# Performance work log

Hardware: AMD Instinct MI355X
Metric: run time of the kernel (lower is better)

Reference implementation:

```python
import jax, jax.numpy as jnp
import numpy as np
import math

D_MODEL = 1024
NUM_HEADS = 16
HEAD_DIM = D_MODEL // NUM_HEADS
THETA = 10000.0
B, S = 2, 2048


def _rope(x, positions, theta):
    # x: (b, h, s, d); positions: (s,) int
    d = x.shape[-1]
    inv_freq = theta ** (-jnp.arange(0, d, 2, dtype=jnp.float32) / d)  # (d/2,)
    ang = positions.astype(jnp.float32)[:, None] * inv_freq[None, :]   # (s, d/2)
    cos, sin = jnp.cos(ang), jnp.sin(ang)
    x1 = x[..., ::2]
    x2 = x[..., 1::2]
    r1 = x1 * cos - x2 * sin
    r2 = x1 * sin + x2 * cos
    # interleave back to (..., d)
    return jnp.stack([r1, r2], axis=-1).reshape(x.shape)


def setup_inputs() -> dict:
    key = jax.random.key(0)
    ks = jax.random.split(key, 5)
    std = math.sqrt(2.0 / (D_MODEL + D_MODEL))
    return {
        "x": jax.random.normal(ks[0], (B, S, D_MODEL), dtype=jnp.float32),
        "token_positions": jnp.arange(S, dtype=jnp.int32),
        "Wq": jax.random.normal(ks[1], (D_MODEL, D_MODEL), dtype=jnp.float32) * std,
        "Wk": jax.random.normal(ks[2], (D_MODEL, D_MODEL), dtype=jnp.float32) * std,
        "Wv": jax.random.normal(ks[3], (D_MODEL, D_MODEL), dtype=jnp.float32) * std,
        "Wo": jax.random.normal(ks[4], (D_MODEL, D_MODEL), dtype=jnp.float32) * std,
    }


def reference(x, token_positions, Wq, Wk, Wv, Wo):
    b, s, _ = x.shape
    def split_heads(t):
        return t.reshape(b, s, NUM_HEADS, HEAD_DIM).transpose(0, 2, 1, 3)  # (b,h,s,d)
    Q = split_heads(x @ Wq.T)
    K = split_heads(x @ Wk.T)
    V = split_heads(x @ Wv.T)
    Q = _rope(Q, token_positions, THETA)
    K = _rope(K, token_positions, THETA)
    scores = jnp.einsum("bhqd,bhkd->bhqk", Q, K) / math.sqrt(HEAD_DIM)
    causal = jnp.tril(jnp.ones((s, s), dtype=bool))
    scores = jnp.where(causal, scores, -jnp.inf)
    attn = jax.nn.softmax(scores, axis=-1)
    out = jnp.einsum("bhqk,bhkd->bhqd", attn, V)
    out = out.transpose(0, 2, 1, 3).reshape(b, s, D_MODEL)
    return out @ Wo.T
```

## Files before the change

### kernel.cpp

```cpp
#include <hip/hip_runtime.h>
#include <math.h>

typedef unsigned short u16;
typedef unsigned int   u32;
typedef __attribute__((ext_vector_type(8))) short bf16x8;
typedef __attribute__((ext_vector_type(4))) float floatx4;
typedef __attribute__((ext_vector_type(4))) _Float16 halfx4;
typedef __attribute__((ext_vector_type(2))) unsigned int uintx2;

#define SEQ 2048
#define DM  1024
#define NH  16
#define DH  64
#define MM  4096
#define QSCALE 0.18033688011112042f

__device__ __forceinline__ u16 f2bf(float f) {
    u32 u = __builtin_bit_cast(u32, f);
    u += 0x7fffu + ((u >> 16) & 1u);
    return (u16)(u >> 16);
}

__device__ __forceinline__ void async16(const void* g, void* l) {
    __builtin_amdgcn_global_load_lds(
        (const __attribute__((address_space(1))) void*)g,
        (__attribute__((address_space(3))) void*)l, 16, 0, 0);
}

__global__ __launch_bounds__(256) void prep_kernel(const float* __restrict__ x,
                                                   const float* __restrict__ w0,
                                                   const float* __restrict__ w1,
                                                   const float* __restrict__ w2,
                                                   const float* __restrict__ w3,
                                                   u16* __restrict__ Xsh,
                                                   u16* __restrict__ Wsh,
                                                   const int* __restrict__ pos,
                                                   float2* __restrict__ tab) {
    const int bid = blockIdx.x, cb = blockIdx.y, tid = threadIdx.x;

    int lin = bid * 16 + cb;
    if (lin < 256) {
        int i = lin * 256 + tid;
        int p = i >> 5, d2 = i & 31;
        float freq = __expf(-(float)d2 * (9.2103403719761836f / 32.0f));
        float sv, cv;
        sincosf((float)pos[p] * freq, &sv, &cv);
        tab[i] = make_float2(cv, sv);
    }

    const float* src; u16* dst; int row0;
    if (bid < 64) { src = x; dst = Xsh; row0 = bid * 64; }
    else {
        int wi = (bid - 64) >> 4;
        src = (wi == 0) ? w0 : (wi == 1) ? w1 : (wi == 2) ? w2 : w3;
        dst = Wsh + (size_t)wi * DM * DM;
        row0 = ((bid - 64) & 15) * 64;
    }
    __shared__ __align__(16) u16 t[64 * 64];
#pragma unroll
    for (int rep = 0; rep < 4; ++rep) {
        int f = rep * 256 + tid;
        int r = f >> 4, c4 = f & 15;
        float4 v = *(const float4*)&src[(size_t)(row0 + r) * DM + cb * 64 + c4 * 4];
        uint2 pk;
        pk.x = (u32)f2bf(v.x) | ((u32)f2bf(v.y) << 16);
        pk.y = (u32)f2bf(v.z) | ((u32)f2bf(v.w) << 16);
        int ch = (c4 >> 1) ^ (r & 7);
        *(uint2*)&t[r * 64 + ch * 8 + (c4 & 1) * 4] = pk;
    }
    __syncthreads();
#pragma unroll
    for (int rep = 0; rep < 2; ++rep) {
        int s = rep * 256 + tid;
        int tile = s >> 6, l = s & 63;
        int mt = tile >> 1, kt = tile & 1, lm = l & 15, quad = l >> 4;
        int m = mt * 16 + lm;
        uint4 v = *(const uint4*)&t[m * 64 + ((kt * 4 + quad) ^ (m & 7)) * 8];
        size_t rowblk = (size_t)(row0 >> 4) + mt;
        size_t ktile  = cb * 2 + kt;
        *(uint4*)&dst[(rowblk * 32 + ktile) * 512 + l * 8] = v;
    }
}

template<int MREP, bool OUTF32>
__global__ __launch_bounds__(256, (MREP == 4) ? 3 : 2)
void gemm_s(const u16* __restrict__ Ash,
            const u16* __restrict__ Wbase,
            u16* __restrict__ qout,
            float* __restrict__ outf,
            _Float16* __restrict__ vtout,
            u16* __restrict__ kout,
            const float2* __restrict__ ropetab) {
    constexpr int BM  = MREP * 32;
    constexpr int AC  = 2 * MREP;
    constexpr int APW = AC / 4;
    constexpr int STEP = (AC + 8) * 512;
    constexpr int SHN  = (MREP == 4) ? (128 * 136) : (2 * STEP);

    const int z  = blockIdx.z;
    const u16* Wp = Wbase + (size_t)z * (DM * DM);
    const int m0 = blockIdx.x * BM, n0 = blockIdx.y * 128;
    const int tid = threadIdx.x, lane = tid & 63, w = tid >> 6;
    const int wr = w >> 1, wc = w & 1;
    const int lm = lane & 15, quad = lane >> 4;
    const int rb0 = m0 >> 4, cb0 = n0 >> 4;

    __shared__ __align__(16) u16 sh[SHN];

    auto stage = [&](int buf, int it) {
        u16* la = sh + buf * STEP;
        u16* lb = la + AC * 512;
#pragma unroll
        for (int j = 0; j < APW; ++j) {
            int c = w * APW + j;
            async16(Ash + ((size_t)(rb0 + c) * 32 + it) * 512 + lane * 8,
                    &la[c * 512 + lane * 8]);
        }
#pragma unroll
        for (int j = 0; j < 2; ++j) {
            int c = w * 2 + j;
            async16(Wp + ((size_t)(cb0 + c) * 32 + it) * 512 + lane * 8,
                    &lb[c * 512 + lane * 8]);
        }
    };

    floatx4 acc[MREP][4];
    const floatx4 z4 = {0.f, 0.f, 0.f, 0.f};
#pragma unroll
    for (int mt = 0; mt < MREP; ++mt)
#pragma unroll
        for (int nt = 0; nt < 4; ++nt) acc[mt][nt] = z4;

    stage(0, 0);
    __syncthreads();

#pragma unroll 2
    for (int it = 0; it < 32; ++it) {
        if (it < 31) stage((it + 1) & 1, it + 1);
        const u16* la = sh + (it & 1) * STEP;
        const u16* lb = la + AC * 512;
        bf16x8 a[MREP], b[4];
#pragma unroll
        for (int mt = 0; mt < MREP; ++mt)
            a[mt] = *(const bf16x8*)&la[(wr * MREP + mt) * 512 + lane * 8];
#pragma unroll
        for (int nt = 0; nt < 4; ++nt)
            b[nt] = *(const bf16x8*)&lb[(wc * 4 + nt) * 512 + lane * 8];
#pragma unroll
        for (int mt = 0; mt < MREP; ++mt)
#pragma unroll
            for (int nt = 0; nt < 4; ++nt)
                acc[mt][nt] = __builtin_amdgcn_mfma_f32_16x16x32_bf16(
                    a[mt], b[nt], acc[mt][nt], 0, 0, 0);
        __syncthreads();
    }

    if constexpr (OUTF32) {
#pragma unroll
        for (int mt = 0; mt < MREP; ++mt)
#pragma unroll
            for (int r = 0; r < 4; ++r) {
                int row = m0 + wr * (MREP * 16) + mt * 16 + quad * 4 + r;
#pragma unroll
                for (int nt = 0; nt < 4; ++nt) {
                    int col = n0 + wc * 64 + nt * 16 + lm;
                    outf[(size_t)row * DM + col] = acc[mt][nt][r];
                }
            }
        return;
    } else {
        if (z == 0) {
#pragma unroll
            for (int mt = 0; mt < MREP; ++mt)
#pragma unroll
                for (int r = 0; r < 4; ++r) {
                    int row = m0 + wr * (MREP * 16) + mt * 16 + quad * 4 + r;
#pragma unroll
                    for (int nt = 0; nt < 4; ++nt) {
                        int col = n0 + wc * 64 + nt * 16 + lm;
                        float v  = acc[mt][nt][r];
                        float pv = __shfl_xor(v, 1);
                        float2 cs = ropetab[(row & (SEQ - 1)) * 32 + ((col & 63) >> 1)];
                        v = (lm & 1) ? fmaf(pv, cs.y, v * cs.x) : fmaf(v, cs.x, -pv * cs.y);
                        v *= QSCALE;
                        float hv = __shfl_xor(v, 1);
                        if (!(lm & 1)) {
                            u32 pk = (u32)f2bf(v) | ((u32)f2bf(hv) << 16);
                            *(u32*)&qout[(size_t)row * DM + col] = pk;
                        }
                    }
                }
        } else if (z == 1) {
            if constexpr (MREP == 4) {
                u16* t = sh;
#pragma unroll
                for (int mt = 0; mt < MREP; ++mt)
#pragma unroll
                    for (int r = 0; r < 4; ++r) {
                        int rl  = wr * 64 + mt * 16 + quad * 4 + r;
                        int row = m0 + rl;
#pragma unroll
                        for (int nt = 0; nt < 4; ++nt) {
                            int cl  = wc * 64 + nt * 16 + lm;
                            int col = n0 + cl;
                            float v  = acc[mt][nt][r];
                            float pv = __shfl_xor(v, 1);
                            float2 cs = ropetab[(row & (SEQ - 1)) * 32 + ((col & 63) >> 1)];
                            v = (lm & 1) ? fmaf(pv, cs.y, v * cs.x) : fmaf(v, cs.x, -pv * cs.y);
                            t[rl * 136 + cl] = f2bf(v);
                        }
                    }
                __syncthreads();
                {
                    int bb = m0 >> 11;
                    int sblk0 = (m0 & (SEQ - 1)) >> 4;
                    int h0 = n0 >> 6;
#pragma unroll
                    for (int j = 0; j < 8; ++j) {
                        int c = w * 8 + j;
                        int hloc = c >> 4, sblkl = (c >> 1) & 7, ks2 = c & 1;
                        uint4 v4 = *(const uint4*)&t[(sblkl * 16 + lm) * 136 + hloc * 64 + ks2 * 32 + quad * 8];
                        size_t chunk = ((size_t)(bb * NH + h0 + hloc) * 128 + sblk0 + sblkl) * 2 + ks2;
                        *(uint4*)&kout[chunk * 512 + lane * 8] = v4;
                    }
                }
            }
        } else {
            if constexpr (MREP == 4) {
#pragma unroll
                for (int mt = 0; mt < MREP; ++mt) {
                    int row = m0 + wr * 64 + mt * 16;
                    int b = row >> 11;
                    int sblk = (row & (SEQ - 1)) >> 4;
#pragma unroll
                    for (int nt = 0; nt < 4; ++nt) {
                        int col = n0 + wc * 64 + nt * 16;
                        int h = col >> 6;
                        int dblk = (col & 63) >> 4;
                        size_t chunk = ((size_t)(b * NH + h) * 128 + sblk) * 4 + dblk;
                        uint2 pk;
                        pk.x = __builtin_bit_cast(u32, __builtin_amdgcn_cvt_pkrtz(acc[mt][nt][0], acc[mt][nt][1]));
                        pk.y = __builtin_bit_cast(u32, __builtin_amdgcn_cvt_pkrtz(acc[mt][nt][2], acc[mt][nt][3]));
                        *(uint2*)&vtout[chunk * 256 + lane * 4] = pk;
                    }
                }
            }
        }
    }
}

__global__ __launch_bounds__(256, 2) void attn_kernel(const u16* __restrict__ Q,
                                                      const u16* __restrict__ Kf,
                                                      const _Float16* __restrict__ Vf,
                                                      u16* __restrict__ AO) {
    const int u  = blockIdx.x;
    const int qt = (u < 256) ? (15 - (u >> 5)) : ((u >> 5) - 8);
    const int bh = u & 31;
    const int b  = bh >> 4, h = bh & 15;
    const int q0 = qt * 128;
    const int tid = threadIdx.x, w = tid >> 6, lane = tid & 63;
    const int lm = lane & 15, quad = lane >> 4;

    __shared__ __align__(16) u16      lsK[2][16 * 512];
    __shared__ __align__(16) _Float16 lsV[2][32 * 256];

    bf16x8 qb[2][2];
#pragma unroll
    for (int qi = 0; qi < 2; ++qi)
#pragma unroll
        for (int ks = 0; ks < 2; ++ks)
            qb[qi][ks] = *(const bf16x8*)
                &Q[(size_t)(b * SEQ + q0 + w * 32 + qi * 16 + lm) * DM + h * DH + ks * 32 + quad * 8];

    const floatx4 z4 = {0.f, 0.f, 0.f, 0.f};
    floatx4 o[2][4];
    floatx4 o5[2];
#pragma unroll
    for (int qi = 0; qi < 2; ++qi) {
#pragma unroll
        for (int dt = 0; dt < 4; ++dt) o[qi][dt] = z4;
        o5[qi] = z4;
    }

    const u16*      Kb = Kf + (size_t)bh * (256 * 512);
    const _Float16* Vb = Vf + (size_t)bh * (128 * 4 * 256);

    auto stageKV = [&](int buf, int kt) {
#pragma unroll
        for (int j = 0; j < 4; ++j) {
            int kc = w * 4 + j;
            async16(Kb + ((size_t)kt * 16 + kc) * 512 + lane * 8,
                    &lsK[buf][kc * 512 + lane * 8]);
            int off = w * 2048 + j * 512 + lane * 8;
            async16(Vb + (size_t)kt * 8192 + off, &lsV[buf][off]);
        }
    };

    stageKV(0, 0);
    const halfx4 ones = {(_Float16)1.f, (_Float16)1.f, (_Float16)1.f, (_Float16)1.f};

    for (int kt = 0; kt <= qt; ++kt) {
        __syncthreads();
        if (kt < qt) stageKV((kt + 1) & 1, kt + 1);
        const u16*      Lk = lsK[kt & 1];
        const _Float16* Lv = lsV[kt & 1];

        floatx4 s4[2][8];
#pragma unroll
        for (int qi = 0; qi < 2; ++qi)
#pragma unroll
            for (int st = 0; st < 8; ++st) s4[qi][st] = z4;
#pragma unroll
        for (int ks = 0; ks < 2; ++ks)
#pragma unroll
            for (int st = 0; st < 8; ++st) {
                bf16x8 ka = *(const bf16x8*)&Lk[(st * 2 + ks) * 512 + lane * 8];
#pragma unroll
                for (int qi = 0; qi < 2; ++qi)
                    s4[qi][st] = __builtin_amdgcn_mfma_f32_16x16x32_bf16(ka, qb[qi][ks], s4[qi][st], 0, 0, 0);
            }

        const bool diag = (kt == qt);
#pragma unroll
        for (int st = 0; st < 8; ++st) {
            halfx4 pb2[2];
#pragma unroll
            for (int qi = 0; qi < 2; ++qi) {
#pragma unroll
                for (int r = 0; r < 4; ++r) {
                    float v = s4[qi][st][r];
                    if (diag) {
                        int keyloc = st * 16 + quad * 4 + r;
                        if (keyloc > w * 32 + qi * 16 + lm) v = -1e30f;
                    }
                    s4[qi][st][r] = exp2f(v);
                }
                uintx2 pk2;
                pk2.x = __builtin_bit_cast(u32, __builtin_amdgcn_cvt_pkrtz(s4[qi][st][0], s4[qi][st][1]));
                pk2.y = __builtin_bit_cast(u32, __builtin_amdgcn_cvt_pkrtz(s4[qi][st][2], s4[qi][st][3]));
                pb2[qi] = __builtin_bit_cast(halfx4, pk2);
            }
#pragma unroll
            for (int dt = 0; dt < 4; ++dt) {
                halfx4 va = *(const halfx4*)&Lv[(st * 4 + dt) * 256 + lane * 4];
#pragma unroll
                for (int qi = 0; qi < 2; ++qi)
                    o[qi][dt] = __builtin_amdgcn_mfma_f32_16x16x16f16(va, pb2[qi], o[qi][dt], 0, 0, 0);
            }
#pragma unroll
            for (int qi = 0; qi < 2; ++qi)
                o5[qi] = __builtin_amdgcn_mfma_f32_16x16x16f16(ones, pb2[qi], o5[qi], 0, 0, 0);
        }
    }

    float rl[2] = {1.0f / o5[0][0], 1.0f / o5[1][0]};

    __syncthreads();
    u16* eb = (u16*)&lsK[0][0];
#pragma unroll
    for (int qi = 0; qi < 2; ++qi) {
        const int q = w * 32 + qi * 16 + lm;
#pragma unroll
        for (int dt = 0; dt < 4; ++dt) {
            uint2 pk;
            pk.x = (u32)f2bf(o[qi][dt][0] * rl[qi]) | ((u32)f2bf(o[qi][dt][1] * rl[qi]) << 16);
            pk.y = (u32)f2bf(o[qi][dt][2] * rl[qi]) | ((u32)f2bf(o[qi][dt][3] * rl[qi]) << 16);
            int ch = (dt * 2 + (quad >> 1)) ^ (lm & 7);
            *(uint2*)&eb[q * 64 + ch * 8 + (quad & 1) * 4] = pk;
        }
    }
    __syncthreads();
    const size_t rowblk0 = (size_t)((b * SEQ + q0) >> 4);
#pragma unroll
    for (int rbi = 0; rbi < 2; ++rbi) {
#pragma unroll
        for (int kt = 0; kt < 2; ++kt) {
            uint4 v = *(const uint4*)&eb[((w * 2 + rbi) * 16 + lm) * 64 + ((kt * 4 + quad) ^ (lm & 7)) * 8];
            *(uint4*)&AO[((rowblk0 + w * 2 + rbi) * 32 + (h * 2 + kt)) * 512 + lane * 8] = v;
        }
    }
}

extern "C" void kernel_launch(void* const* d_in, const int* in_sizes, int n_in,
                              void* d_out, int out_size, void* d_ws, size_t ws_size,
                              hipStream_t stream) {
    const float* x   = (const float*)d_in[0];
    const int*   pos = (const int*)d_in[1];
    float* out = (float*)d_out;

    u16* ws = (u16*)d_ws;
    const size_t MD = (size_t)MM * DM;
    const size_t DD = (size_t)DM * DM;
    u16* Xsh = ws;
    u16* Wsh = ws + MD;
    u16* Qbf = ws + MD + 4 * DD;
    u16* Kfb = Qbf + MD;
    u16* VtB = Kfb + MD;
    float2* ropetab = (float2*)(VtB + MD);
    _Float16* Vt = (_Float16*)VtB;
    u16* AOsh = Xsh;

    prep_kernel<<<dim3(128, 16), 256, 0, stream>>>(
        x, (const float*)d_in[2], (const float*)d_in[3], (const float*)d_in[4],
        (const float*)d_in[5], Xsh, Wsh, pos, ropetab);

    gemm_s<4, false><<<dim3(32, 8, 3), 256, 0, stream>>>(
        Xsh, Wsh, Qbf, nullptr, Vt, Kfb, ropetab);

    attn_kernel<<<dim3(512), 256, 0, stream>>>(Qbf, Kfb, Vt, AOsh);

    gemm_s<2, true><<<dim3(64, 8, 1), 256, 0, stream>>>(
        AOsh, Wsh + 3 * DD, nullptr, out, nullptr, nullptr, ropetab);
}
```

Before: 179.5 us.

## Split KV range of longest causal query tiles and merge with combine kernel

The attention grid grows from 512 to 672 blocks. A lookup table maps each block to a query tile and a key-tile range. The five longest causal query tiles (qt 11–15) are split into two key-range halves. Each half writes unnormalized fp16 partial outputs and row sums into spare workspace, and a new combine kernel adds the two halves, normalizes and writes the bf16 attention output. The aim is to shorten the critical path set by the longest tiles and balance work across CUs. The cost is an extra launch, partial-result traffic and fp16 rounding of the partials. exp2f is also swapped for the hardware exp2 builtin.

```diff
diff --git a/kernel.cpp b/kernel.cpp
--- a/kernel.cpp
+++ b/kernel.cpp
@@ -6,6 +6,7 @@
 typedef __attribute__((ext_vector_type(8))) short bf16x8;
 typedef __attribute__((ext_vector_type(4))) float floatx4;
 typedef __attribute__((ext_vector_type(4))) _Float16 halfx4;
+typedef __attribute__((ext_vector_type(8))) _Float16 halfx8;
 typedef __attribute__((ext_vector_type(2))) unsigned int uintx2;
 
 #define SEQ 2048
@@ -249,13 +250,30 @@
     }
 }
 
+static __device__ const u16 itab[21] = {
+    0x0B0A,
+    0x0A09,
+    0x0908,
+    0x280F, 0x708F, 0x6F7E, 0x0807,
+    0x270E, 0x270D, 0x6E7D, 0x6D6C, 0x0706,
+    0x260C, 0x260B, 0x6C6B, 0x0605,
+    0x0504, 0x0403, 0x0302, 0x0201, 0x0100
+};
+
 __global__ __launch_bounds__(256, 2) void attn_kernel(const u16* __restrict__ Q,
                                                       const u16* __restrict__ Kf,
                                                       const _Float16* __restrict__ Vf,
-                                                      u16* __restrict__ AO) {
+                                                      u16* __restrict__ AO,
+                                                      _Float16* __restrict__ Opart,
+                                                      float* __restrict__ Lpart) {
     const int u  = blockIdx.x;
-    const int qt = (u < 256) ? (15 - (u >> 5)) : ((u >> 5) - 8);
+    const int e  = itab[u >> 5];
     const int bh = u & 31;
+    const int qt = e & 15;
+    const int k0 = (e >> 4) & 15;
+    const int k1 = (e >> 8) & 31;
+    const bool split = (e >> 13) & 1;
+    const int part = e >> 14;
     const int b  = bh >> 4, h = bh & 15;
     const int q0 = qt * 128;
     const int tid = threadIdx.x, w = tid >> 6, lane = tid & 63;
@@ -296,12 +314,12 @@
         }
     };
 
-    stageKV(0, 0);
+    stageKV(k0 & 1, k0);
     const halfx4 ones = {(_Float16)1.f, (_Float16)1.f, (_Float16)1.f, (_Float16)1.f};
 
-    for (int kt = 0; kt <= qt; ++kt) {
+    for (int kt = k0; kt < k1; ++kt) {
         __syncthreads();
-        if (kt < qt) stageKV((kt + 1) & 1, kt + 1);
+        if (kt + 1 < k1) stageKV((kt + 1) & 1, kt + 1);
         const u16*      Lk = lsK[kt & 1];
         const _Float16* Lv = lsV[kt & 1];
 
@@ -333,7 +351,7 @@
                         int keyloc = st * 16 + quad * 4 + r;
                         if (keyloc > w * 32 + qi * 16 + lm) v = -1e30f;
                     }
-                    s4[qi][st][r] = exp2f(v);
+                    s4[qi][st][r] = __builtin_amdgcn_exp2f(v);
                 }
                 uintx2 pk2;
                 pk2.x = __builtin_bit_cast(u32, __builtin_amdgcn_cvt_pkrtz(s4[qi][st][0], s4[qi][st][1]));
@@ -351,6 +369,24 @@
             for (int qi = 0; qi < 2; ++qi)
                 o5[qi] = __builtin_amdgcn_mfma_f32_16x16x16f16(ones, pb2[qi], o5[qi], 0, 0, 0);
         }
+    }
+
+    if (split) {
+        const int pi = (bh * 5 + (qt - 11)) * 2 + part;
+        _Float16* Od = Opart + (size_t)pi * (128 * 64);
+#pragma unroll
+        for (int qi = 0; qi < 2; ++qi) {
+            const int q = w * 32 + qi * 16 + lm;
+#pragma unroll
+            for (int dt = 0; dt < 4; ++dt) {
+                uintx2 pk2;
+                pk2.x = __builtin_bit_cast(u32, __builtin_amdgcn_cvt_pkrtz(o[qi][dt][0], o[qi][dt][1]));
+                pk2.y = __builtin_bit_cast(u32, __builtin_amdgcn_cvt_pkrtz(o[qi][dt][2], o[qi][dt][3]));
+                *(uintx2*)&Od[(size_t)q * 64 + dt * 16 + quad * 4] = pk2;
+            }
+            if (quad == 0) Lpart[pi * 128 + q] = o5[qi][0];
+        }
+        return;
     }
 
     float rl[2] = {1.0f / o5[0][0], 1.0f / o5[1][0]};
@@ -378,6 +414,45 @@
             uint4 v = *(const uint4*)&eb[((w * 2 + rbi) * 16 + lm) * 64 + ((kt * 4 + quad) ^ (lm & 7)) * 8];
             *(uint4*)&AO[((rowblk0 + w * 2 + rbi) * 32 + (h * 2 + kt)) * 512 + lane * 8] = v;
         }
+    }
+}
+
+__global__ __launch_bounds__(256) void combine_kernel(const _Float16* __restrict__ Op,
+                                                      const float* __restrict__ Lp,
+                                                      u16* __restrict__ AO) {
+    const int g = blockIdx.x;
+    const int bh = g / 5, qto = g - bh * 5;
+    const int qt = 11 + qto;
+    const int b = bh >> 4, h = bh & 15;
+    const int q0 = qt * 128;
+    const int pi0 = g * 2;
+    const _Float16* O0 = Op + (size_t)pi0 * (128 * 64);
+    const _Float16* O1 = O0 + 128 * 64;
+    const float* L0 = Lp + pi0 * 128;
+    const float* L1 = L0 + 128;
+    const int tid = threadIdx.x;
+#pragma unroll
+    for (int rep = 0; rep < 4; ++rep) {
+        int idx = rep * 256 + tid;
+        int chunk = idx >> 6, lane = idx & 63;
+        int rb = chunk >> 1, kt2 = chunk & 1;
+        int lm = lane & 15, quad = lane >> 4;
+        int q = rb * 16 + lm;
+        int d = kt2 * 32 + quad * 8;
+        float rl = 1.0f / (L0[q] + L1[q]);
+        halfx8 a = *(const halfx8*)&O0[(size_t)q * 64 + d];
+        halfx8 c = *(const halfx8*)&O1[(size_t)q * 64 + d];
+        uint4 v;
+        u32 pk[4];
+#pragma unroll
+        for (int j = 0; j < 4; ++j) {
+            float v0 = ((float)a[2 * j]     + (float)c[2 * j])     * rl;
+            float v1 = ((float)a[2 * j + 1] + (float)c[2 * j + 1]) * rl;
+            pk[j] = (u32)f2bf(v0) | ((u32)f2bf(v1) << 16);
+        }
+        v.x = pk[0]; v.y = pk[1]; v.z = pk[2]; v.w = pk[3];
+        size_t rowblk = ((size_t)(b * SEQ + q0) >> 4) + rb;
+        *(uint4*)&AO[(rowblk * 32 + (h * 2 + kt2)) * 512 + lane * 8] = v;
     }
 }
 
@@ -399,6 +474,8 @@
     float2* ropetab = (float2*)(VtB + MD);
     _Float16* Vt = (_Float16*)VtB;
     u16* AOsh = Xsh;
+    _Float16* Opart = (_Float16*)Wsh;
+    float* Lpart = (float*)(ropetab + SEQ * 32);
 
     prep_kernel<<<dim3(128, 16), 256, 0, stream>>>(
         x, (const float*)d_in[2], (const float*)d_in[3], (const float*)d_in[4],
@@ -407,7 +484,9 @@
     gemm_s<4, false><<<dim3(32, 8, 3), 256, 0, stream>>>(
         Xsh, Wsh, Qbf, nullptr, Vt, Kfb, ropetab);
 
-    attn_kernel<<<dim3(512), 256, 0, stream>>>(Qbf, Kfb, Vt, AOsh);
+    attn_kernel<<<dim3(672), 256, 0, stream>>>(Qbf, Kfb, Vt, AOsh, Opart, Lpart);
+
+    combine_kernel<<<dim3(160), 256, 0, stream>>>(Opart, Lpart, AOsh);
 
     gemm_s<2, true><<<dim3(64, 8, 1), 256, 0, stream>>>(
         AOsh, Wsh + 3 * DD, nullptr, out, nullptr, nullptr, ropetab);
```

New measurement: 175.4 us. 2.3% less time.
